# Optimization experiments

Hardware: AMD Instinct MI355X
Metric: run time of the kernel (lower is better)

Reference implementation:

```python
import jax, jax.numpy as jnp
import numpy as np

N_EMBD = 1024
NUM_HEADS = 16
HEAD_SIZE = 64


def setup_inputs() -> dict:
    key = jax.random.key(0)
    ks = jax.random.split(key, 6)
    B, T, C, hs = 2, 2048, N_EMBD, HEAD_SIZE
    s = 0.02
    return {
        "x": jax.random.normal(ks[0], (B, T, C), dtype=jnp.float32),
        "Wk": jax.random.normal(ks[1], (hs, C), dtype=jnp.float32) * s,  # torch Linear weight [out,in]
        "Wv": jax.random.normal(ks[2], (hs, C), dtype=jnp.float32) * s,
        "Wq": jax.random.normal(ks[3], (C, C), dtype=jnp.float32) * s,
        "Wp": jax.random.normal(ks[4], (C, C), dtype=jnp.float32) * s,
        "bp": jax.random.normal(ks[5], (C,), dtype=jnp.float32) * s,
    }


def reference(x, Wk, Wv, Wq, Wp, bp):
    B, T, C = x.shape
    H, hs = NUM_HEADS, HEAD_SIZE
    k = x @ Wk.T                      # [B,T,hs]
    v = x @ Wv.T                      # [B,T,hs]
    q = x @ Wq.T                      # [B,T,C]
    # Faithful to torch: raw view of [B,T,C] -> [B,H,T,hs] (row-major reshape, not transpose)
    q = q.reshape(B, H, T, hs)
    k = k.reshape(B, 1, T, hs)
    v = v.reshape(B, 1, T, hs)
    att = jnp.einsum("bhqd,bhkd->bhqk", q, jnp.broadcast_to(k, (B, 1, T, hs))) * (hs ** -0.5)
    mask = jnp.tril(jnp.ones((T, T), dtype=bool))[None, None]  # [1,1,T,T]
    att = jnp.where(mask, att, -jnp.inf)
    att = jax.nn.softmax(att, axis=-1)
    y = jnp.einsum("bhqk,bhkd->bhqd", att, jnp.broadcast_to(v, (B, 1, T, hs)))  # [B,H,T,hs]
    y = jnp.transpose(y, (0, 2, 1, 3)).reshape(B, T, C)
    return y @ Wp.T + bp
```

## Files before the change

kernel.cpp:

```cpp
#include <hip/hip_runtime.h>
#include <cstddef>
#include <cstdint>

#define B_N 2
#define T_N 2048
#define C_N 1024
#define H_N 16
#define HS_N 64
#define M_N (B_N * T_N)

typedef __attribute__((ext_vector_type(8))) short bf16x8;
typedef __attribute__((ext_vector_type(4))) float f32x4;

#define QSCALE 0.18033688011112042f

__device__ __forceinline__ ushort f2bf(float f) {
    union { float f; uint32_t u; } v; v.f = f;
    uint32_t r = v.u + 0x7fffu + ((v.u >> 16) & 1u);
    return (ushort)(r >> 16);
}

#define GLL16(g, l)                                                         \
    __builtin_amdgcn_global_load_lds(                                       \
        (const __attribute__((address_space(1))) unsigned int*)(g),         \
        (__attribute__((address_space(3))) unsigned int*)(l), 16, 0, 0)

__global__ void cvt_all_kernel(const float* __restrict__ x,
                               const float* __restrict__ Wq,
                               const float* __restrict__ Wp,
                               const float* __restrict__ Wk,
                               const float* __restrict__ Wv,
                               ushort* __restrict__ xb,
                               ushort* __restrict__ Wqb,
                               ushort* __restrict__ Wpb,
                               ushort* __restrict__ Wkvb) {
    const int S0 = M_N * C_N / 4;
    const int S1 = S0 + C_N * C_N / 4;
    const int S2 = S1 + C_N * C_N / 4;
    const int S3 = S2 + HS_N * C_N / 4;
    const int S4 = S3 + HS_N * C_N / 4;
    const int stride = gridDim.x * blockDim.x;
    for (int i = blockIdx.x * blockDim.x + threadIdx.x; i < S4; i += stride) {
        const float* src; ushort* dst; int j; float sc = 1.f;
        if (i < S0)      { src = x;  dst = xb;   j = i; }
        else if (i < S1) { src = Wq; dst = Wqb;  j = i - S0; sc = QSCALE; }
        else if (i < S2) { src = Wp; dst = Wpb;  j = i - S1; }
        else if (i < S3) { src = Wk; dst = Wkvb; j = i - S2; }
        else             { src = Wv; dst = Wkvb + HS_N * C_N; j = i - S3; }
        const float4 f = ((const float4*)src)[j];
        ushort4 o;
        o.x = f2bf(f.x * sc); o.y = f2bf(f.y * sc);
        o.z = f2bf(f.z * sc); o.w = f2bf(f.w * sc);
        ((ushort4*)dst)[j] = o;
    }
}

template <int MODE>
__global__ __launch_bounds__(256) void gemm64(
    const ushort* __restrict__ A,
    const ushort* __restrict__ W,
    const float* __restrict__ bias,
    void* __restrict__ Cout,
    ushort* __restrict__ kb,
    ushort* __restrict__ vbt,
    int K)
{
    __shared__ ushort As[64 * 64];
    __shared__ ushort Bs[64 * 64];
    const int m0 = blockIdx.x * 64;
    const int n0 = blockIdx.y * 64;
    const int tid = threadIdx.x;
    const int wid = tid >> 6;
    const int lane = tid & 63;
    const int ln = lane & 15;
    const int quad = lane >> 4;
    const int wm = wid >> 1, wn = wid & 1;

    f32x4 acc[2][2];
    #pragma unroll
    for (int i = 0; i < 2; ++i)
        #pragma unroll
        for (int j = 0; j < 2; ++j)
            acc[i][j] = (f32x4){0.f, 0.f, 0.f, 0.f};

    const int srow = lane >> 3;
    const int schk = (lane & 7) ^ srow;

    for (int k0 = 0; k0 < K; k0 += 64) {
        __syncthreads();
        #pragma unroll
        for (int t = 0; t < 2; ++t) {
            const int seg = wid * 2 + t;
            GLL16(A + (size_t)(m0 + seg * 8 + srow) * K + k0 + schk * 8,
                  As + seg * 512);
        }
        #pragma unroll
        for (int t = 0; t < 2; ++t) {
            const int seg = wid * 2 + t;
            GLL16(W + (size_t)(n0 + seg * 8 + srow) * K + k0 + schk * 8,
                  Bs + seg * 512);
        }
        __syncthreads();

        #pragma unroll
        for (int hh = 0; hh < 2; ++hh) {
            bf16x8 af[2], bf[2];
            const int sw = ln & 7;
            #pragma unroll
            for (int i = 0; i < 2; ++i) {
                const int row = wm * 32 + i * 16 + ln;
                af[i] = *(const bf16x8*)&As[row * 64 + (((hh * 4 + quad) ^ sw) * 8)];
            }
            #pragma unroll
            for (int j = 0; j < 2; ++j) {
                const int row = wn * 32 + j * 16 + ln;
                bf[j] = *(const bf16x8*)&Bs[row * 64 + (((hh * 4 + quad) ^ sw) * 8)];
            }
            #pragma unroll
            for (int i = 0; i < 2; ++i)
                #pragma unroll
                for (int j = 0; j < 2; ++j)
                    acc[i][j] = __builtin_amdgcn_mfma_f32_16x16x32_bf16(
                        af[i], bf[j], acc[i][j], 0, 0, 0);
        }
    }

    if (MODE == 1 && n0 >= C_N) {
        const int c2base = n0 - C_N;
        const bool isV = (c2base >= 64);
        #pragma unroll
        for (int i = 0; i < 2; ++i) {
            const int row0 = m0 + wm * 32 + i * 16 + quad * 4;
            #pragma unroll
            for (int j = 0; j < 2; ++j) {
                const int c2 = c2base + wn * 32 + j * 16 + ln;
                if (isV) {
                    const int d = c2 - 64;
                    const int b = row0 >> 11;
                    const int t0 = row0 & 2047;
                    ushort4 pk;
                    pk.x = f2bf(acc[i][j][0]); pk.y = f2bf(acc[i][j][1]);
                    pk.z = f2bf(acc[i][j][2]); pk.w = f2bf(acc[i][j][3]);
                    *(ushort4*)&vbt[((size_t)b * 64 + d) * T_N + t0] = pk;
                } else {
                    #pragma unroll
                    for (int reg = 0; reg < 4; ++reg)
                        kb[(size_t)(row0 + reg) * 64 + c2] = f2bf(acc[i][j][reg]);
                }
            }
        }
        return;
    }

    #pragma unroll
    for (int i = 0; i < 2; ++i) {
        #pragma unroll
        for (int j = 0; j < 2; ++j) {
            const int col = n0 + wn * 32 + j * 16 + ln;
            const float bv = (MODE == 0) ? bias[col] : 0.f;
            #pragma unroll
            for (int reg = 0; reg < 4; ++reg) {
                const int row = m0 + wm * 32 + i * 16 + quad * 4 + reg;
                const float v = acc[i][j][reg] + bv;
                if (MODE == 0)
                    ((float*)Cout)[(size_t)row * C_N + col] = v;
                else
                    ((ushort*)Cout)[(size_t)row * C_N + col] = f2bf(v);
            }
        }
    }
}

__global__ __launch_bounds__(256, 2) void attn_mfma_kernel(
    const ushort* __restrict__ qb,
    const ushort* __restrict__ kb,
    const ushort* __restrict__ vbt,
    ushort* __restrict__ yb)
{
    __shared__ ushort Ks[64][72];
    __shared__ ushort Vt[64][72];
    __shared__ ushort Ps[4][16][72];

    const int bh = blockIdx.x;
    const int b = bh >> 4, h = bh & 15;
    const int p = blockIdx.y;
    const int qA0 = p * 64;
    const int qB0 = (31 - p) * 64;
    const int tid = threadIdx.x;
    const int wid = tid >> 6;
    const int lane = tid & 63;
    const int ln = lane & 15;
    const int quad = lane >> 4;

    const ushort* qstrip = qb + (size_t)b * T_N * C_N + (size_t)h * T_N * HS_N;
    const size_t rB = (size_t)(qB0 + wid * 16 + ln) * HS_N;
    const size_t rA = (size_t)(qA0 + wid * 16 + ln) * HS_N;
    bf16x8 qfB[2], qfA[2];
    qfB[0] = *(const bf16x8*)(qstrip + rB + quad * 8);
    qfB[1] = *(const bf16x8*)(qstrip + rB + 32 + quad * 8);
    qfA[0] = *(const bf16x8*)(qstrip + rA + quad * 8);
    qfA[1] = *(const bf16x8*)(qstrip + rA + 32 + quad * 8);

    f32x4 oB[4], oA[4];
    float lB = 0.f, lA = 0.f;
    #pragma unroll
    for (int nt = 0; nt < 4; ++nt) {
        oB[nt] = (f32x4){0.f, 0.f, 0.f, 0.f};
        oA[nt] = (f32x4){0.f, 0.f, 0.f, 0.f};
    }

    const ushort* kbase = kb + (size_t)b * T_N * HS_N;
    const ushort* vtbase = vbt + (size_t)b * HS_N * T_N;
    const int rs = tid >> 3;
    const int cs = tid & 7;

    int4 kc0, kc1, vc0, vc1;
    {
        kc0 = *(const int4*)(kbase + (size_t)rs * HS_N + cs * 8);
        kc1 = *(const int4*)(kbase + (size_t)(rs + 32) * HS_N + cs * 8);
        vc0 = *(const int4*)(vtbase + (size_t)rs * T_N + cs * 8);
        vc1 = *(const int4*)(vtbase + (size_t)(rs + 32) * T_N + cs * 8);
    }

    bf16x8 kf[4][2], vf[4][2];

    auto tile_compute = [&](const bf16x8* qf, f32x4* o, float& l,
                            int qt0, int k0) {
        const int qs0 = qt0 + wid * 16;
        const int qg = qs0 + ln;
        f32x4 sc[4];
        #pragma unroll
        for (int nt = 0; nt < 4; ++nt) {
            sc[nt] = (f32x4){0.f, 0.f, 0.f, 0.f};
            sc[nt] = __builtin_amdgcn_mfma_f32_16x16x32_bf16(
                kf[nt][0], qf[0], sc[nt], 0, 0, 0);
            sc[nt] = __builtin_amdgcn_mfma_f32_16x16x32_bf16(
                kf[nt][1], qf[1], sc[nt], 0, 0, 0);
        }
        const bool dg = (k0 + 63 > qs0);
        #pragma unroll
        for (int nt = 0; nt < 4; ++nt) {
            ushort pk[4];
            #pragma unroll
            for (int reg = 0; reg < 4; ++reg) {
                const int key = k0 + nt * 16 + quad * 4 + reg;
                float sv = sc[nt][reg];
                if (dg && key > qg) sv = -1e30f;
                const float pe = __builtin_amdgcn_exp2f(sv);
                l += pe;
                pk[reg] = f2bf(pe);
            }
            *(uint2*)&Ps[wid][ln][nt * 16 + quad * 4] = *(const uint2*)pk;
        }
        #pragma unroll
        for (int ks2 = 0; ks2 < 2; ++ks2) {
            const bf16x8 pf = *(const bf16x8*)&Ps[wid][ln][ks2 * 32 + quad * 8];
            #pragma unroll
            for (int nt = 0; nt < 4; ++nt)
                o[nt] = __builtin_amdgcn_mfma_f32_16x16x32_bf16(
                    pf, vf[nt][ks2], o[nt], 0, 0, 0);
        }
    };

    const int nkt = 32 - p;
    for (int kt = 0; kt < nkt; ++kt) {
        const int k0 = kt * 64;
        __syncthreads();
        *(int4*)&Ks[rs][cs * 8] = kc0;
        *(int4*)&Ks[rs + 32][cs * 8] = kc1;
        *(int4*)&Vt[rs][cs * 8] = vc0;
        *(int4*)&Vt[rs + 32][cs * 8] = vc1;
        __syncthreads();
        if (kt + 1 < nkt) {
            const int kn = k0 + 64;
            kc0 = *(const int4*)(kbase + (size_t)(kn + rs) * HS_N + cs * 8);
            kc1 = *(const int4*)(kbase + (size_t)(kn + rs + 32) * HS_N + cs * 8);
            vc0 = *(const int4*)(vtbase + (size_t)rs * T_N + kn + cs * 8);
            vc1 = *(const int4*)(vtbase + (size_t)(rs + 32) * T_N + kn + cs * 8);
        }
        #pragma unroll
        for (int nt = 0; nt < 4; ++nt) {
            kf[nt][0] = *(const bf16x8*)&Ks[nt * 16 + ln][quad * 8];
            kf[nt][1] = *(const bf16x8*)&Ks[nt * 16 + ln][32 + quad * 8];
            vf[nt][0] = *(const bf16x8*)&Vt[nt * 16 + ln][quad * 8];
            vf[nt][1] = *(const bf16x8*)&Vt[nt * 16 + ln][32 + quad * 8];
        }
        tile_compute(qfB, oB, lB, qB0, k0);
        if (kt <= p)
            tile_compute(qfA, oA, lA, qA0, k0);
    }

    #pragma unroll
    for (int t = 0; t < 2; ++t) {
        float l = t ? lA : lB;
        const f32x4* o = t ? oA : oB;
        const int qt0 = t ? qA0 : qB0;
        l += __shfl_xor(l, 16);
        l += __shfl_xor(l, 32);
        #pragma unroll
        for (int reg = 0; reg < 4; ++reg) {
            const float inv = 1.0f / __shfl(l, quad * 4 + reg);
            const int qg = qt0 + wid * 16 + quad * 4 + reg;
            ushort* yrow = yb + (size_t)b * T_N * C_N + (size_t)qg * C_N
                           + h * HS_N;
            #pragma unroll
            for (int nt = 0; nt < 4; ++nt)
                yrow[nt * 16 + ln] = f2bf(o[nt][reg] * inv);
        }
    }
}

extern "C" void kernel_launch(void* const* d_in, const int* in_sizes, int n_in,
                              void* d_out, int out_size, void* d_ws, size_t ws_size,
                              hipStream_t stream) {
    const float* x  = (const float*)d_in[0];
    const float* Wk = (const float*)d_in[1];
    const float* Wv = (const float*)d_in[2];
    const float* Wq = (const float*)d_in[3];
    const float* Wp = (const float*)d_in[4];
    const float* bp = (const float*)d_in[5];
    float* out = (float*)d_out;

    ushort* xb   = (ushort*)d_ws;
    ushort* qb   = xb   + (size_t)M_N * C_N;
    ushort* yb   = qb   + (size_t)M_N * C_N;
    ushort* kbw  = yb   + (size_t)M_N * C_N;
    ushort* vbt  = kbw  + (size_t)M_N * HS_N;
    ushort* Wqb  = vbt  + (size_t)B_N * HS_N * T_N;
    ushort* Wkvb = Wqb  + (size_t)C_N * C_N;
    ushort* Wpb  = Wkvb + (size_t)128 * C_N;

    cvt_all_kernel<<<1024, 256, 0, stream>>>(x, Wq, Wp, Wk, Wv,
                                             xb, Wqb, Wpb, Wkvb);

    gemm64<1><<<dim3(M_N / 64, (C_N + 128) / 64), 256, 0, stream>>>(
        xb, Wqb, nullptr, qb, kbw, vbt, C_N);

    attn_mfma_kernel<<<dim3(B_N * H_N, 16), 256, 0, stream>>>(qb, kbw, vbt, yb);

    gemm64<0><<<dim3(M_N / 64, C_N / 64), 256, 0, stream>>>(
        yb, Wpb, bp, out, nullptr, nullptr, C_N);
}
```

Measured before the change: 154.3 us.

## Widen GEMM tiles to 64x128 and double-buffer K/V tiles in attention

The GEMM kernels now compute a 64x128 output tile per block, with each wave holding a 32x64 accumulator region. This halves the number of blocks and reuses each A tile across twice as many columns, at the cost of more registers and LDS per block. The attention kernel double-buffers its K/V shared-memory tiles so the next tile is written while the current one is consumed, which removes one barrier per iteration. The trade-offs are higher register and LDS pressure and fewer blocks to fill the GPU.

```diff
diff --git a/kernel.cpp b/kernel.cpp
--- a/kernel.cpp
+++ b/kernel.cpp
@@ -56,7 +56,7 @@
 }
 
 template <int MODE>
-__global__ __launch_bounds__(256) void gemm64(
+__global__ __launch_bounds__(256, 2) void gemm_bf16(
     const ushort* __restrict__ A,
     const ushort* __restrict__ W,
     const float* __restrict__ bias,
@@ -66,9 +66,9 @@
     int K)
 {
     __shared__ ushort As[64 * 64];
-    __shared__ ushort Bs[64 * 64];
+    __shared__ ushort Bs[128 * 64];
     const int m0 = blockIdx.x * 64;
-    const int n0 = blockIdx.y * 64;
+    const int n0 = blockIdx.y * 128;
     const int tid = threadIdx.x;
     const int wid = tid >> 6;
     const int lane = tid & 63;
@@ -76,11 +76,11 @@
     const int quad = lane >> 4;
     const int wm = wid >> 1, wn = wid & 1;
 
-    f32x4 acc[2][2];
+    f32x4 acc[2][4];
     #pragma unroll
     for (int i = 0; i < 2; ++i)
         #pragma unroll
-        for (int j = 0; j < 2; ++j)
+        for (int j = 0; j < 4; ++j)
             acc[i][j] = (f32x4){0.f, 0.f, 0.f, 0.f};
 
     const int srow = lane >> 3;
@@ -95,8 +95,8 @@
                   As + seg * 512);
         }
         #pragma unroll
-        for (int t = 0; t < 2; ++t) {
-            const int seg = wid * 2 + t;
+        for (int t = 0; t < 4; ++t) {
+            const int seg = wid * 4 + t;
             GLL16(W + (size_t)(n0 + seg * 8 + srow) * K + k0 + schk * 8,
                   Bs + seg * 512);
         }
@@ -104,7 +104,7 @@
 
         #pragma unroll
         for (int hh = 0; hh < 2; ++hh) {
-            bf16x8 af[2], bf[2];
+            bf16x8 af[2], bf[4];
             const int sw = ln & 7;
             #pragma unroll
             for (int i = 0; i < 2; ++i) {
@@ -112,29 +112,27 @@
                 af[i] = *(const bf16x8*)&As[row * 64 + (((hh * 4 + quad) ^ sw) * 8)];
             }
             #pragma unroll
-            for (int j = 0; j < 2; ++j) {
-                const int row = wn * 32 + j * 16 + ln;
+            for (int j = 0; j < 4; ++j) {
+                const int row = wn * 64 + j * 16 + ln;
                 bf[j] = *(const bf16x8*)&Bs[row * 64 + (((hh * 4 + quad) ^ sw) * 8)];
             }
             #pragma unroll
             for (int i = 0; i < 2; ++i)
                 #pragma unroll
-                for (int j = 0; j < 2; ++j)
+                for (int j = 0; j < 4; ++j)
                     acc[i][j] = __builtin_amdgcn_mfma_f32_16x16x32_bf16(
                         af[i], bf[j], acc[i][j], 0, 0, 0);
         }
     }
 
     if (MODE == 1 && n0 >= C_N) {
-        const int c2base = n0 - C_N;
-        const bool isV = (c2base >= 64);
         #pragma unroll
         for (int i = 0; i < 2; ++i) {
             const int row0 = m0 + wm * 32 + i * 16 + quad * 4;
             #pragma unroll
-            for (int j = 0; j < 2; ++j) {
-                const int c2 = c2base + wn * 32 + j * 16 + ln;
-                if (isV) {
+            for (int j = 0; j < 4; ++j) {
+                const int c2 = wn * 64 + j * 16 + ln;
+                if (c2 >= 64) {
                     const int d = c2 - 64;
                     const int b = row0 >> 11;
                     const int t0 = row0 & 2047;
@@ -155,8 +153,8 @@
     #pragma unroll
     for (int i = 0; i < 2; ++i) {
         #pragma unroll
-        for (int j = 0; j < 2; ++j) {
-            const int col = n0 + wn * 32 + j * 16 + ln;
+        for (int j = 0; j < 4; ++j) {
+            const int col = n0 + wn * 64 + j * 16 + ln;
             const float bv = (MODE == 0) ? bias[col] : 0.f;
             #pragma unroll
             for (int reg = 0; reg < 4; ++reg) {
@@ -177,8 +175,8 @@
     const ushort* __restrict__ vbt,
     ushort* __restrict__ yb)
 {
-    __shared__ ushort Ks[64][72];
-    __shared__ ushort Vt[64][72];
+    __shared__ ushort Ks[2][64][72];
+    __shared__ ushort Vt[2][64][72];
     __shared__ ushort Ps[4][16][72];
 
     const int bh = blockIdx.x;
@@ -214,13 +212,26 @@
     const int rs = tid >> 3;
     const int cs = tid & 7;
 
+    const int nkt = 32 - p;
+
     int4 kc0, kc1, vc0, vc1;
     {
         kc0 = *(const int4*)(kbase + (size_t)rs * HS_N + cs * 8);
         kc1 = *(const int4*)(kbase + (size_t)(rs + 32) * HS_N + cs * 8);
         vc0 = *(const int4*)(vtbase + (size_t)rs * T_N + cs * 8);
         vc1 = *(const int4*)(vtbase + (size_t)(rs + 32) * T_N + cs * 8);
-    }
+        *(int4*)&Ks[0][rs][cs * 8] = kc0;
+        *(int4*)&Ks[0][rs + 32][cs * 8] = kc1;
+        *(int4*)&Vt[0][rs][cs * 8] = vc0;
+        *(int4*)&Vt[0][rs + 32][cs * 8] = vc1;
+    }
+    if (nkt > 1) {
+        kc0 = *(const int4*)(kbase + (size_t)(64 + rs) * HS_N + cs * 8);
+        kc1 = *(const int4*)(kbase + (size_t)(64 + rs + 32) * HS_N + cs * 8);
+        vc0 = *(const int4*)(vtbase + (size_t)rs * T_N + 64 + cs * 8);
+        vc1 = *(const int4*)(vtbase + (size_t)(rs + 32) * T_N + 64 + cs * 8);
+    }
+    __syncthreads();
 
     bf16x8 kf[4][2], vf[4][2];
 
@@ -262,17 +273,17 @@
         }
     };
 
-    const int nkt = 32 - p;
     for (int kt = 0; kt < nkt; ++kt) {
         const int k0 = kt * 64;
-        __syncthreads();
-        *(int4*)&Ks[rs][cs * 8] = kc0;
-        *(int4*)&Ks[rs + 32][cs * 8] = kc1;
-        *(int4*)&Vt[rs][cs * 8] = vc0;
-        *(int4*)&Vt[rs + 32][cs * 8] = vc1;
-        __syncthreads();
+        const int cur = kt & 1, nxt = cur ^ 1;
         if (kt + 1 < nkt) {
-            const int kn = k0 + 64;
+            *(int4*)&Ks[nxt][rs][cs * 8] = kc0;
+            *(int4*)&Ks[nxt][rs + 32][cs * 8] = kc1;
+            *(int4*)&Vt[nxt][rs][cs * 8] = vc0;
+            *(int4*)&Vt[nxt][rs + 32][cs * 8] = vc1;
+        }
+        if (kt + 2 < nkt) {
+            const int kn = k0 + 128;
             kc0 = *(const int4*)(kbase + (size_t)(kn + rs) * HS_N + cs * 8);
             kc1 = *(const int4*)(kbase + (size_t)(kn + rs + 32) * HS_N + cs * 8);
             vc0 = *(const int4*)(vtbase + (size_t)rs * T_N + kn + cs * 8);
@@ -280,14 +291,15 @@
         }
         #pragma unroll
         for (int nt = 0; nt < 4; ++nt) {
-            kf[nt][0] = *(const bf16x8*)&Ks[nt * 16 + ln][quad * 8];
-            kf[nt][1] = *(const bf16x8*)&Ks[nt * 16 + ln][32 + quad * 8];
-            vf[nt][0] = *(const bf16x8*)&Vt[nt * 16 + ln][quad * 8];
-            vf[nt][1] = *(const bf16x8*)&Vt[nt * 16 + ln][32 + quad * 8];
+            kf[nt][0] = *(const bf16x8*)&Ks[cur][nt * 16 + ln][quad * 8];
+            kf[nt][1] = *(const bf16x8*)&Ks[cur][nt * 16 + ln][32 + quad * 8];
+            vf[nt][0] = *(const bf16x8*)&Vt[cur][nt * 16 + ln][quad * 8];
+            vf[nt][1] = *(const bf16x8*)&Vt[cur][nt * 16 + ln][32 + quad * 8];
         }
         tile_compute(qfB, oB, lB, qB0, k0);
         if (kt <= p)
             tile_compute(qfA, oA, lA, qA0, k0);
+        __syncthreads();
     }
 
     #pragma unroll
@@ -333,11 +345,11 @@
     cvt_all_kernel<<<1024, 256, 0, stream>>>(x, Wq, Wp, Wk, Wv,
                                              xb, Wqb, Wpb, Wkvb);
 
-    gemm64<1><<<dim3(M_N / 64, (C_N + 128) / 64), 256, 0, stream>>>(
+    gemm_bf16<1><<<dim3(M_N / 64, (C_N + 128) / 128), 256, 0, stream>>>(
         xb, Wqb, nullptr, qb, kbw, vbt, C_N);
 
     attn_mfma_kernel<<<dim3(B_N * H_N, 16), 256, 0, stream>>>(qb, kbw, vbt, yb);
 
-    gemm64<0><<<dim3(M_N / 64, C_N / 64), 256, 0, stream>>>(
+    gemm_bf16<0><<<dim3(M_N / 64, C_N / 128), 256, 0, stream>>>(
         yb, Wpb, bp, out, nullptr, nullptr, C_N);
 }
```

Result: no change. 155.1 us (+0.5%).
